# Kernel optimization log

Measured on AMD Instinct MI355X. Metric: run time of the kernel, lower is better.

## Reference

```python
import jax, jax.numpy as jnp
from jax import lax
import numpy as np

B, CIN, COUT, WDIM, RES = 8, 512, 512, 512, 64


def setup_inputs() -> dict:
    key = jax.random.key(0)
    k0, k1, k2, k3 = jax.random.split(key, 4)
    x = jax.random.normal(k0, (B, CIN, RES, RES), dtype=jnp.float32)
    w = jax.random.normal(k1, (B, WDIM), dtype=jnp.float32)
    weight = jax.random.normal(k2, (COUT, CIN, 3, 3), dtype=jnp.float32)
    bias = jnp.zeros((COUT,), dtype=jnp.float32)
    affine_w = jax.random.normal(k3, (CIN, WDIM), dtype=jnp.float32) * 0.02
    affine_b = jnp.zeros((CIN,), dtype=jnp.float32)
    return {"x": x, "w": w, "weight": weight, "bias": bias,
            "affine_w": affine_w, "affine_b": affine_b}


def reference(x, w, weight, bias, affine_w, affine_b):
    # style: [B, Cin] = affine(w)
    style = w @ affine_w.T + affine_b
    b, cin, h, wd = x.shape
    cout = weight.shape[0]
    # per-sample modulated weight: [B, Cout, Cin, 3, 3]
    wmod = weight[None, :, :, :, :] * style[:, None, :, None, None]
    # grouped conv with groups = batch: lhs [1, B*Cin, H, W], rhs [B*Cout, Cin, 3, 3]
    lhs = x.reshape(1, b * cin, h, wd)
    rhs = wmod.reshape(b * cout, cin, 3, 3)
    y = lax.conv_general_dilated(
        lhs, rhs,
        window_strides=(1, 1),
        padding=[(1, 1), (1, 1)],
        dimension_numbers=("NCHW", "OIHW", "NCHW"),
        feature_group_count=b,
    )
    y = y.reshape(b, cout, h, wd)
    return y + bias[None, :, None, None]
```

## Files before the change

### kernel.cpp

```cpp
#include <hip/hip_runtime.h>
#include <cstdint>
#include <cstddef>

#define BATCH 8
#define CIN   512
#define COUT  512
#define RES   64
#define HW    4096
#define WDIM  512

typedef short bf16x8 __attribute__((ext_vector_type(8)));
typedef float f32x4  __attribute__((ext_vector_type(4)));
typedef unsigned short ushort8 __attribute__((ext_vector_type(8)));

typedef const __attribute__((address_space(1))) void* gas_ptr;
typedef __attribute__((address_space(3))) void*       las_ptr;

__device__ __forceinline__ unsigned short f2bf(float f) {
    unsigned int u = __float_as_uint(f);
    u += 0x7fffu + ((u >> 16) & 1u);
    return (unsigned short)(u >> 16);
}

__global__ __launch_bounds__(256) void prep_kernel(
    const float* __restrict__ w, const float* __restrict__ aw,
    const float* __restrict__ ab, float* __restrict__ style,
    unsigned short* __restrict__ zpage,
    const float* __restrict__ wt, unsigned short* __restrict__ wr)
{
    __shared__ float buf[4608];
    int bid = blockIdx.x;
    int t = threadIdx.x;
    if (bid < 1024) {
        if (bid == 0 && t < 128) zpage[t] = 0;
        int wv = t >> 6, lane = t & 63;
        int idx = bid * 4 + wv;
        int b = idx >> 9, ci = idx & 511;
        const float* wrow = w + b * WDIM;
        const float* arow = aw + (size_t)ci * WDIM;
        float s = 0.f;
#pragma unroll
        for (int i = 0; i < WDIM / 64; ++i) s += arow[lane + i * 64] * wrow[lane + i * 64];
#pragma unroll
        for (int off = 32; off; off >>= 1) s += __shfl_down(s, off);
        if (lane == 0) style[idx] = s + ab[ci];
    } else {
        int co = bid - 1024;
#pragma unroll
        for (int r = 0; r < 18; ++r) buf[r * 256 + t] = wt[(size_t)co * 4608 + r * 256 + t];
        __syncthreads();
#pragma unroll
        for (int r = 0; r < 18; ++r) {
            int idx = r * 256 + t;
            int tap = idx >> 9, ci = idx & 511;
            wr[(size_t)tap * (COUT * CIN) + co * CIN + ci] = f2bf(buf[ci * 9 + tap]);
        }
    }
}

__global__ __launch_bounds__(256) void modtrans_kernel(
    const float* __restrict__ x, const float* __restrict__ style,
    unsigned short* __restrict__ xs)
{
    __shared__ float tile[64][65];
    int t = threadIdx.x;
    int hw0 = blockIdx.x * 64, ci0 = blockIdx.y * 64, b = blockIdx.z;
    int sub = t >> 6, lane = t & 63;
#pragma unroll
    for (int r = 0; r < 16; ++r) {
        int ci = r * 4 + sub;
        float s = style[b * CIN + ci0 + ci];
        tile[ci][lane] = x[((size_t)(b * CIN + ci0 + ci)) * HW + hw0 + lane] * s;
    }
    __syncthreads();
    int ci8 = (t & 7) * 8;
#pragma unroll
    for (int r = 0; r < 2; ++r) {
        int hw = r * 32 + (t >> 3);
        ushort8 v;
#pragma unroll
        for (int j = 0; j < 8; ++j) v[j] = f2bf(tile[ci8 + j][hw]);
        *(ushort8*)&xs[((size_t)b * HW + hw0 + hw) * CIN + ci0 + ci8] = v;
    }
}

__global__ __launch_bounds__(256) void conv_kernel(
    const unsigned short* __restrict__ xs,
    const unsigned short* __restrict__ wr,
    const float* __restrict__ bias,
    const unsigned short* __restrict__ zpage,
    float* __restrict__ y)
{
    __shared__ __align__(16) unsigned short As[3 * 128 * 32];
    __shared__ __align__(16) unsigned short Bs[2 * 66 * 32];

    const int t   = threadIdx.x;
    const int bid = blockIdx.x;
    const int co0 = (bid >> 8) * 128;
    const int rem = bid & 255;
    const int h0  = (rem >> 3) * 2;
    const int b   = rem & 7;

    const int lane = t & 63;
    const int wv   = t >> 6;
    const int wm   = (wv & 1) * 64;
    const int wn   = (wv >> 1) * 64;
    const int r16  = lane & 15;
    const int quad = lane >> 4;

    if (t < 128) {
        int d = t >> 6, c = t & 63;
        int col = (c < 32) ? 0 : 65;
        Bs[(d * 66 + col) * 32 + (c & 31)] = 0;
    }

    f32x4 acc[4][4];
#pragma unroll
    for (int mi = 0; mi < 4; ++mi)
#pragma unroll
        for (int ni = 0; ni < 4; ++ni)
            acc[mi][ni] = (f32x4){0.f, 0.f, 0.f, 0.f};

    for (int kh = 0; kh < 3; ++kh) {
        const unsigned short* pA[6];
#pragma unroll
        for (int L = 0; L < 6; ++L) {
            int lin = L * 256 + t;
            int tap = kh * 3 + (lin >> 9);
            int q   = (lin >> 2) & 127;
            int c8  = ((lin & 3) ^ ((lin >> 3) & 3)) * 8;
            pA[L] = wr + (size_t)tap * (COUT * CIN) + (co0 + q) * CIN + c8;
        }
        const unsigned short* pB[2];
        int sB[2];
#pragma unroll
        for (int L = 0; L < 2; ++L) {
            int lin = L * 256 + t;
            int dh = lin >> 8, r8 = lin & 255;
            int wc = r8 >> 2;
            int rowp = dh * 66 + 1 + wc;
            int c8 = ((r8 & 3) ^ ((rowp >> 1) & 3)) * 8;
            int hp = h0 + dh + kh - 1;
            bool ok = (unsigned)hp < 64u;
            pB[L] = ok ? xs + ((size_t)b * HW + hp * 64 + wc) * CIN + c8 : zpage;
            sB[L] = ok ? 32 : 0;
        }

        for (int ch = 0; ch < 16; ++ch) {
#pragma unroll
            for (int L = 0; L < 6; ++L) {
                int lin = L * 256 + t;
                __builtin_amdgcn_global_load_lds((gas_ptr)pA[L], (las_ptr)&As[lin * 8], 16, 0, 0);
                pA[L] += 32;
            }
#pragma unroll
            for (int L = 0; L < 2; ++L) {
                int lin = L * 256 + t;
                int dh = lin >> 8, r8 = lin & 255;
                __builtin_amdgcn_global_load_lds((gas_ptr)pB[L],
                    (las_ptr)&Bs[(dh * 66 + 1) * 32 + r8 * 8], 16, 0, 0);
                pB[L] += sB[L];
            }
            __syncthreads();
#pragma unroll
            for (int kw = 0; kw < 3; ++kw) {
                bf16x8 af[4], bfv[4];
#pragma unroll
                for (int mi = 0; mi < 4; ++mi) {
                    int row = kw * 128 + wm + mi * 16 + r16;
                    int ck  = quad ^ ((row >> 1) & 3);
                    af[mi] = *(const bf16x8*)&As[row * 32 + ck * 8];
                }
#pragma unroll
                for (int ni = 0; ni < 4; ++ni) {
                    int n = wn + ni * 16 + r16;
                    int dh = n >> 6, wc = n & 63;
                    int row = dh * 66 + wc + kw;
                    int ck  = quad ^ ((row >> 1) & 3);
                    bfv[ni] = *(const bf16x8*)&Bs[row * 32 + ck * 8];
                }
#pragma unroll
                for (int mi = 0; mi < 4; ++mi)
#pragma unroll
                    for (int ni = 0; ni < 4; ++ni)
                        acc[mi][ni] = __builtin_amdgcn_mfma_f32_16x16x32_bf16(
                            af[mi], bfv[ni], acc[mi][ni], 0, 0, 0);
            }
            __syncthreads();
        }
    }

#pragma unroll
    for (int mi = 0; mi < 4; ++mi) {
#pragma unroll
        for (int r = 0; r < 4; ++r) {
            int m = co0 + wm + mi * 16 + quad * 4 + r;
            float bv = bias[m];
            size_t base = ((size_t)b * COUT + m) * HW + h0 * 64;
#pragma unroll
            for (int ni = 0; ni < 4; ++ni) {
                int n = wn + ni * 16 + r16;
                y[base + n] = acc[mi][ni][r] + bv;
            }
        }
    }
}

extern "C" void kernel_launch(void* const* d_in, const int* in_sizes, int n_in,
                              void* d_out, int out_size, void* d_ws, size_t ws_size,
                              hipStream_t stream)
{
    (void)in_sizes; (void)n_in; (void)out_size; (void)ws_size;
    const float* x    = (const float*)d_in[0];
    const float* w    = (const float*)d_in[1];
    const float* wt   = (const float*)d_in[2];
    const float* bias = (const float*)d_in[3];
    const float* aw   = (const float*)d_in[4];
    const float* ab   = (const float*)d_in[5];
    float* y = (float*)d_out;

    char* ws = (char*)d_ws;
    float*          style = (float*)ws;
    unsigned short* zpage = (unsigned short*)(ws + 16384);
    unsigned short* wr    = (unsigned short*)(ws + 32768);
    unsigned short* xs    = (unsigned short*)(ws + 4751360);

    prep_kernel<<<1536, 256, 0, stream>>>(w, aw, ab, style, zpage, wt, wr);
    modtrans_kernel<<<dim3(64, 8, 8), 256, 0, stream>>>(x, style, xs);
    conv_kernel<<<1024, 256, 0, stream>>>(xs, wr, bias, zpage, y);
}
```

Baseline: 265.2 us.

## Double-buffer LDS tiles in conv kernel to overlap loads with MFMA

Doubles the A and B shared-memory tiles and flattens the kh/ch loops into a single 48-step loop. The next chunk's global-to-LDS loads are issued before the current chunk's MFMAs, and there is one barrier per step instead of two. MFMA sections are wrapped in s_setprio to favour matrix issue. LDS use roughly doubles, which may lower occupancy. There is also a possible hazard: the async LDS loads may not be waited on before the barrier, since there is no explicit vmcnt wait.

```diff
diff --git a/kernel.cpp b/kernel.cpp
--- a/kernel.cpp
+++ b/kernel.cpp
@@ -91,8 +91,10 @@
     const unsigned short* __restrict__ zpage,
     float* __restrict__ y)
 {
-    __shared__ __align__(16) unsigned short As[3 * 128 * 32];
-    __shared__ __align__(16) unsigned short Bs[2 * 66 * 32];
+    __shared__ __align__(16) unsigned short As[2 * 3 * 128 * 32];
+    __shared__ __align__(16) unsigned short Bs[2 * 2 * 66 * 32];
+    constexpr int ABUF = 3 * 128 * 32;
+    constexpr int BBUF = 2 * 66 * 32;
 
     const int t   = threadIdx.x;
     const int bid = blockIdx.x;
@@ -108,10 +110,12 @@
     const int r16  = lane & 15;
     const int quad = lane >> 4;
 
-    if (t < 128) {
-        int d = t >> 6, c = t & 63;
+    {
+        int bufz = t >> 7;
+        int r = t & 127;
+        int d = r >> 6, c = r & 63;
         int col = (c < 32) ? 0 : 65;
-        Bs[(d * 66 + col) * 32 + (c & 31)] = 0;
+        Bs[bufz * BBUF + (d * 66 + col) * 32 + (c & 31)] = 0;
     }
 
     f32x4 acc[4][4];
@@ -121,8 +125,11 @@
         for (int ni = 0; ni < 4; ++ni)
             acc[mi][ni] = (f32x4){0.f, 0.f, 0.f, 0.f};
 
-    for (int kh = 0; kh < 3; ++kh) {
-        const unsigned short* pA[6];
+    const unsigned short* pA[6];
+    const unsigned short* pB[2];
+    int sB[2];
+
+    auto setup = [&](int kh) {
 #pragma unroll
         for (int L = 0; L < 6; ++L) {
             int lin = L * 256 + t;
@@ -131,8 +138,6 @@
             int c8  = ((lin & 3) ^ ((lin >> 3) & 3)) * 8;
             pA[L] = wr + (size_t)tap * (COUT * CIN) + (co0 + q) * CIN + c8;
         }
-        const unsigned short* pB[2];
-        int sB[2];
 #pragma unroll
         for (int L = 0; L < 2; ++L) {
             int lin = L * 256 + t;
@@ -145,48 +150,65 @@
             pB[L] = ok ? xs + ((size_t)b * HW + hp * 64 + wc) * CIN + c8 : zpage;
             sB[L] = ok ? 32 : 0;
         }
-
-        for (int ch = 0; ch < 16; ++ch) {
-#pragma unroll
-            for (int L = 0; L < 6; ++L) {
-                int lin = L * 256 + t;
-                __builtin_amdgcn_global_load_lds((gas_ptr)pA[L], (las_ptr)&As[lin * 8], 16, 0, 0);
-                pA[L] += 32;
+    };
+
+    auto stage = [&](int buf) {
+        const int ab = buf * ABUF, bb = buf * BBUF;
+#pragma unroll
+        for (int L = 0; L < 6; ++L) {
+            int lin = L * 256 + t;
+            __builtin_amdgcn_global_load_lds((gas_ptr)pA[L], (las_ptr)&As[ab + lin * 8], 16, 0, 0);
+            pA[L] += 32;
+        }
+#pragma unroll
+        for (int L = 0; L < 2; ++L) {
+            int lin = L * 256 + t;
+            int dh = lin >> 8, r8 = lin & 255;
+            __builtin_amdgcn_global_load_lds((gas_ptr)pB[L],
+                (las_ptr)&Bs[bb + (dh * 66 + 1) * 32 + r8 * 8], 16, 0, 0);
+            pB[L] += sB[L];
+        }
+    };
+
+    setup(0);
+    stage(0);
+
+    for (int p = 0; p < 48; ++p) {
+        __syncthreads();
+
+        if (p < 47) {
+            int pn = p + 1;
+            if ((pn & 15) == 0) setup(pn >> 4);
+            stage(pn & 1);
+        }
+        __builtin_amdgcn_sched_barrier(0);
+
+        const int ab = (p & 1) * ABUF, bb = (p & 1) * BBUF;
+#pragma unroll
+        for (int kw = 0; kw < 3; ++kw) {
+            bf16x8 af[4], bfv[4];
+#pragma unroll
+            for (int mi = 0; mi < 4; ++mi) {
+                int row = kw * 128 + wm + mi * 16 + r16;
+                int ck  = quad ^ ((row >> 1) & 3);
+                af[mi] = *(const bf16x8*)&As[ab + row * 32 + ck * 8];
             }
 #pragma unroll
-            for (int L = 0; L < 2; ++L) {
-                int lin = L * 256 + t;
-                int dh = lin >> 8, r8 = lin & 255;
-                __builtin_amdgcn_global_load_lds((gas_ptr)pB[L],
-                    (las_ptr)&Bs[(dh * 66 + 1) * 32 + r8 * 8], 16, 0, 0);
-                pB[L] += sB[L];
+            for (int ni = 0; ni < 4; ++ni) {
+                int n = wn + ni * 16 + r16;
+                int dh = n >> 6, wc = n & 63;
+                int row = dh * 66 + wc + kw;
+                int ck  = quad ^ ((row >> 1) & 3);
+                bfv[ni] = *(const bf16x8*)&Bs[bb + row * 32 + ck * 8];
             }
-            __syncthreads();
-#pragma unroll
-            for (int kw = 0; kw < 3; ++kw) {
-                bf16x8 af[4], bfv[4];
-#pragma unroll
-                for (int mi = 0; mi < 4; ++mi) {
-                    int row = kw * 128 + wm + mi * 16 + r16;
-                    int ck  = quad ^ ((row >> 1) & 3);
-                    af[mi] = *(const bf16x8*)&As[row * 32 + ck * 8];
-                }
-#pragma unroll
-                for (int ni = 0; ni < 4; ++ni) {
-                    int n = wn + ni * 16 + r16;
-                    int dh = n >> 6, wc = n & 63;
-                    int row = dh * 66 + wc + kw;
-                    int ck  = quad ^ ((row >> 1) & 3);
-                    bfv[ni] = *(const bf16x8*)&Bs[row * 32 + ck * 8];
-                }
-#pragma unroll
-                for (int mi = 0; mi < 4; ++mi)
-#pragma unroll
-                    for (int ni = 0; ni < 4; ++ni)
-                        acc[mi][ni] = __builtin_amdgcn_mfma_f32_16x16x32_bf16(
-                            af[mi], bfv[ni], acc[mi][ni], 0, 0, 0);
-            }
-            __syncthreads();
+            __builtin_amdgcn_s_setprio(1);
+#pragma unroll
+            for (int mi = 0; mi < 4; ++mi)
+#pragma unroll
+                for (int ni = 0; ni < 4; ++ni)
+                    acc[mi][ni] = __builtin_amdgcn_mfma_f32_16x16x32_bf16(
+                        af[mi], bfv[ni], acc[mi][ni], 0, 0, 0);
+            __builtin_amdgcn_s_setprio(0);
         }
     }
 
```

Result: no change. 264.6 us (-0.2%).
